# Kernel optimization log

Measured on AMD Instinct MI355X. Metric: run time of the kernel, lower is better.

The kernel has to match this reference:

```python
import jax, jax.numpy as jnp
import numpy as np

NUM_CLASSES = 128
MARGIN = 0.1
EPS = 1e-12


def setup_inputs() -> dict:
    key = jax.random.key(0)
    k1, k2, k3, k4, k5 = jax.random.split(key, 5)
    B, D = 32768, 512
    anchor = jax.random.normal(k1, (B, D), dtype=jnp.float32)
    embeddings = jax.random.normal(k2, (B, D), dtype=jnp.float32)
    # SPD inverse-covariance matrix
    A = jax.random.normal(k3, (D, D), dtype=jnp.float32) * 0.05
    cov_inv = A @ A.T + jnp.eye(D, dtype=jnp.float32)
    labels = jax.random.randint(k4, (B,), 0, NUM_CLASSES, dtype=jnp.int32)
    # negative class: deterministic stand-in for the original host-side random.choice,
    # guaranteed different from the anchor class
    offs = jax.random.randint(k5, (B,), 1, NUM_CLASSES, dtype=jnp.int32)
    neg_labels = (labels + offs) % NUM_CLASSES
    return {"anchor": anchor, "embeddings": embeddings, "cov_inv": cov_inv,
            "labels": labels, "neg_labels": neg_labels}


def _mahalanobis(diff, cov_inv):
    # diff: (B, D), cov_inv: (D, D) -> (B,)
    left = diff @ cov_inv
    d2 = jnp.sum(left * diff, axis=-1)
    return jnp.sqrt(jax.nn.relu(d2) + EPS)


def reference(anchor, embeddings, cov_inv, labels, neg_labels):
    B = embeddings.shape[0]
    # class sums / counts once via segment reduce (replaces per-sample masked means)
    sums = jax.ops.segment_sum(embeddings, labels, num_segments=NUM_CLASSES)   # (C, D)
    cnts = jax.ops.segment_sum(jnp.ones((B,), embeddings.dtype), labels,
                               num_segments=NUM_CLASSES)                        # (C,)
    # positive mean of anchor's class, excluding sample i itself
    pos_mean = (sums[labels] - embeddings) / jnp.maximum(cnts[labels] - 1.0, 1.0)[:, None]
    neg_mean = sums[neg_labels] / jnp.maximum(cnts[neg_labels], 1.0)[:, None]
    pos_d = _mahalanobis(anchor - pos_mean, cov_inv)
    neg_d = _mahalanobis(anchor - neg_mean, cov_inv)
    return jnp.mean(jax.nn.relu(pos_d - neg_d + MARGIN))
```

## Files before the change

### kernel.cpp

```cpp
#include <hip/hip_runtime.h>
#include <math.h>

#define D 512
#define C 128
#define B_TOT 32768
#define MARGIN 0.1f
#define EPS 1e-12f

typedef __attribute__((ext_vector_type(4))) short short4v;
typedef __attribute__((ext_vector_type(8))) short short8;
typedef __attribute__((ext_vector_type(16))) float f32x16;

__device__ inline unsigned short f2bf(float f) {
  union { float f; unsigned u; } v; v.f = f;
  unsigned r = v.u + 0x7fff + ((v.u >> 16) & 1);
  return (unsigned short)(r >> 16);
}
__device__ inline float bf2f(unsigned short h) {
  union { unsigned u; float f; } v; v.u = ((unsigned)h) << 16; return v.f;
}

__device__ inline void llds16(void* lds, const void* g) {
  __builtin_amdgcn_global_load_lds(
      (const __attribute__((address_space(1))) unsigned int*)g,
      (__attribute__((address_space(3))) unsigned int*)lds, 16, 0, 0);
}

__global__ __launch_bounds__(256) void prep_m(
    const float* __restrict__ M, unsigned short* __restrict__ Mh,
    float* __restrict__ Mld) {
  int p = blockIdx.x * 4 + (threadIdx.x >> 6);
  int lane = threadIdx.x & 63;
  int s = p >> 4, nt = p & 15;
  int n = nt * 32 + (lane & 31), k0 = s * 16 + (lane >> 5) * 8;
  const float4* mp4 = (const float4*)(M + (size_t)n * D + k0);
  float4 m0 = mp4[0], m1 = mp4[1];
  float mv[8] = {m0.x, m0.y, m0.z, m0.w, m1.x, m1.y, m1.z, m1.w};
  short8 hi;
#pragma unroll
  for (int j = 0; j < 8; ++j) hi[j] = (short)f2bf(mv[j]);
  *(short8*)((char*)Mh + (((size_t)p * 64 + lane) << 4)) = hi;
  if (blockIdx.x == 0) {
    for (int i = threadIdx.x; i < 512; i += 256) {
      float v = M[(size_t)i * 513];
      Mld[i] = v - bf2f(f2bf(v));
    }
  }
}

__global__ __launch_bounds__(256) void seg_part(
    const float* __restrict__ emb, const int* __restrict__ labels,
    float* __restrict__ psum, float* __restrict__ pcnt) {
  int b = blockIdx.x;
  int c = b >> 4, half = (b >> 3) & 1, slice = b & 7;
  int t = threadIdx.x, w = t >> 6, lane = t & 63;
  int col = half * 256 + w * 64 + lane;
  int r0 = slice * 4096;
  float acc = 0.f; int cnt = 0;
  int lab = labels[r0 + lane];
  for (int ch = 0; ch < 64; ++ch) {
    int nxt = (ch < 63) ? labels[r0 + (ch + 1) * 64 + lane] : 0;
    unsigned long long m = __ballot(lab == c);
    cnt += __popcll(m);
    int rb = r0 + ch * 64;
    while (m) {
      int j = __builtin_ctzll(m); m &= m - 1;
      acc += emb[(size_t)(rb + j) * D + col];
    }
    lab = nxt;
  }
  psum[(size_t)(c * 8 + slice) * D + col] = acc;
  if (half == 0 && t == 0) pcnt[c * 8 + slice] = (float)cnt;
}

__global__ __launch_bounds__(256) void seg_reduce(
    const float* __restrict__ psum, const float* __restrict__ pcnt,
    float* __restrict__ sums, float* __restrict__ cnts) {
  int c = blockIdx.x, t = threadIdx.x;
  for (int h = 0; h < 2; ++h) {
    int col = h * 256 + t;
    float s = 0.f;
#pragma unroll
    for (int sl = 0; sl < 8; ++sl) s += psum[(size_t)(c * 8 + sl) * D + col];
    sums[(size_t)c * D + col] = s;
  }
  if (t == 0) {
    float s = 0.f;
    for (int sl = 0; sl < 8; ++sl) s += pcnt[c * 8 + sl];
    cnts[c] = s;
  }
}

__global__ __launch_bounds__(256) void build_x2(
    const float* __restrict__ anchor, const float* __restrict__ emb,
    const int* __restrict__ labels, const int* __restrict__ negl,
    const float* __restrict__ sums, const float* __restrict__ cnts,
    unsigned short* __restrict__ Xfp, unsigned short* __restrict__ Xfn) {
  __shared__ float xsp[32 * 257], xsn[32 * 257];
  const int t = threadIdx.x, w = t >> 6, lane = t & 63;
  const int g = blockIdx.x;
  const int r = lane & 31, koff = (lane >> 5) * 8;

  for (int kh = 0; kh < 2; ++kh) {
    if (kh) __syncthreads();
#pragma unroll 2
    for (int it = 0; it < 8; ++it) {
      int row = it * 4 + w;
      int R = g * 32 + row;
      int lp = labels[R], ln = negl[R];
      float sp = 1.f / fmaxf(cnts[lp] - 1.f, 1.f);
      float sn = 1.f / fmaxf(cnts[ln], 1.f);
      int c0 = kh * 256 + lane * 4;
      float4 a = *(const float4*)(anchor + (size_t)R * D + c0);
      float4 e = *(const float4*)(emb + (size_t)R * D + c0);
      float4 Sp = *(const float4*)(sums + (size_t)lp * D + c0);
      float4 Sn = *(const float4*)(sums + (size_t)ln * D + c0);
      float4 xp, xn;
      xp.x = a.x - sp * (Sp.x - e.x);  xn.x = a.x - sn * Sn.x;
      xp.y = a.y - sp * (Sp.y - e.y);  xn.y = a.y - sn * Sn.y;
      xp.z = a.z - sp * (Sp.z - e.z);  xn.z = a.z - sn * Sn.z;
      xp.w = a.w - sp * (Sp.w - e.w);  xn.w = a.w - sn * Sn.w;
      *(float4*)(xsp + row * 257 + lane * 4) = xp;
      *(float4*)(xsn + row * 257 + lane * 4) = xn;
    }
    __syncthreads();
#pragma unroll
    for (int c = 0; c < 8; ++c) {
      const float* xs = (c < 4) ? xsp : xsn;
      unsigned short* Xf = (c < 4) ? Xfp : Xfn;
      int sl = w * 4 + (c & 3);
      short8 pk;
#pragma unroll
      for (int j = 0; j < 8; ++j)
        pk[j] = (short)f2bf(xs[r * 257 + sl * 16 + koff + j]);
      int s = kh * 16 + sl;
      *(short8*)((char*)Xf + ((((size_t)s * 1024 + g) * 64 + lane) << 4)) = pk;
    }
  }
}

__global__ __launch_bounds__(512, 2) void gemm_d2c(
    const unsigned short* __restrict__ Mh, const float* __restrict__ Mld,
    const unsigned short* __restrict__ Xfp, const unsigned short* __restrict__ Xfn,
    float* __restrict__ d2p) {
  __shared__ char smem[128 * 1024 + 512];
  float* MldL = (float*)(smem + 131072);
  const int t = threadIdx.x, w = t >> 6, lane = t & 63;
  const int chunk = blockIdx.x & 3, rgroup = blockIdx.x >> 2;
  const int isNeg = rgroup >> 6, rg = rgroup & 63;
  const unsigned short* Xsrc = isNeg ? Xfn : Xfp;

#pragma unroll
  for (int c = 0; c < 16; ++c) {
    int idx = w * 16 + c;
    int s = idx >> 2, ntl = idx & 3;
    llds16(smem + idx * 1024,
           (const char*)Mh + ((((size_t)(s * 16 + chunk * 4 + ntl)) * 64 + lane) << 4));
  }
  if (t < 128) MldL[t] = Mld[chunk * 128 + t];
  __syncthreads();

  const int rt0 = rg * 16 + w * 2;
  f32x16 acc[4][2];
#pragma unroll
  for (int nt = 0; nt < 4; ++nt)
#pragma unroll
    for (int rt = 0; rt < 2; ++rt)
#pragma unroll
      for (int i = 0; i < 16; ++i) acc[nt][rt][i] = 0.f;

#pragma unroll
  for (int s = 0; s < 32; ++s) {
    short8 b0 = *(const short8*)((const char*)Xsrc +
        ((((size_t)s * 1024 + rt0) * 64 + lane) << 4));
    short8 b1 = *(const short8*)((const char*)Xsrc +
        ((((size_t)s * 1024 + rt0 + 1) * 64 + lane) << 4));
    short8 a0 = *(const short8*)(smem + ((s * 4 + 0) << 10) + (lane << 4));
    short8 a1 = *(const short8*)(smem + ((s * 4 + 1) << 10) + (lane << 4));
    short8 a2 = *(const short8*)(smem + ((s * 4 + 2) << 10) + (lane << 4));
    short8 a3 = *(const short8*)(smem + ((s * 4 + 3) << 10) + (lane << 4));
    acc[0][0] = __builtin_amdgcn_mfma_f32_32x32x16_bf16(a0, b0, acc[0][0], 0, 0, 0);
    acc[0][1] = __builtin_amdgcn_mfma_f32_32x32x16_bf16(a0, b1, acc[0][1], 0, 0, 0);
    acc[1][0] = __builtin_amdgcn_mfma_f32_32x32x16_bf16(a1, b0, acc[1][0], 0, 0, 0);
    acc[1][1] = __builtin_amdgcn_mfma_f32_32x32x16_bf16(a1, b1, acc[1][1], 0, 0, 0);
    acc[2][0] = __builtin_amdgcn_mfma_f32_32x32x16_bf16(a2, b0, acc[2][0], 0, 0, 0);
    acc[2][1] = __builtin_amdgcn_mfma_f32_32x32x16_bf16(a2, b1, acc[2][1], 0, 0, 0);
    acc[3][0] = __builtin_amdgcn_mfma_f32_32x32x16_bf16(a3, b0, acc[3][0], 0, 0, 0);
    acc[3][1] = __builtin_amdgcn_mfma_f32_32x32x16_bf16(a3, b1, acc[3][1], 0, 0, 0);
  }

  const int rr = lane & 31, lh = lane >> 5;
  float d2l[2];
#pragma unroll
  for (int rt = 0; rt < 2; ++rt) {
    int rtg = rt0 + rt;
    short4v hb[4][2][2];
#pragma unroll
    for (int nt = 0; nt < 4; ++nt)
#pragma unroll
      for (int s2 = 0; s2 < 2; ++s2)
#pragma unroll
        for (int hi = 0; hi < 2; ++hi) {
          int s_h = chunk * 8 + nt * 2 + s2;
          hb[nt][s2][hi] = *(const short4v*)((const char*)Xsrc +
              ((((size_t)s_h * 1024 + rtg) * 64 + hi * 32 + rr) << 4) + lh * 8);
        }
    float d2 = 0.f;
#pragma unroll
    for (int nt = 0; nt < 4; ++nt)
#pragma unroll
      for (int i = 0; i < 16; ++i) {
        float hf = bf2f((unsigned short)hb[nt][i >> 3][(i >> 2) & 1][i & 3]);
        float mld = MldL[nt * 32 + 8 * (i >> 2) + (i & 3) + 4 * lh];
        d2 = fmaf(hf, acc[nt][rt][i] + mld * hf, d2);
      }
    d2l[rt] = d2 + __shfl_xor(d2, 32);
  }
  if (lane < 32) {
    size_t base = (size_t)chunk * 65536 + (size_t)isNeg * 32768 + rg * 512 + w * 64;
#pragma unroll
    for (int rt = 0; rt < 2; ++rt) d2p[base + rt * 32 + rr] = d2l[rt];
  }
}

__global__ __launch_bounds__(256) void loss_partial(
    const float* __restrict__ d2p, int B, float* __restrict__ partial) {
  int i = blockIdx.x * blockDim.x + threadIdx.x;
  float v = 0.f;
  if (i < B) {
    float p2 = 0.f, n2 = 0.f;
#pragma unroll
    for (int c = 0; c < 4; ++c) {
      p2 += d2p[(size_t)c * 65536 + i];
      n2 += d2p[(size_t)c * 65536 + 32768 + i];
    }
    float dp = sqrtf(fmaxf(p2, 0.f) + EPS);
    float dn = sqrtf(fmaxf(n2, 0.f) + EPS);
    v = fmaxf(dp - dn + MARGIN, 0.f);
  }
  for (int off = 32; off; off >>= 1) v += __shfl_down(v, off);
  __shared__ float ws[4];
  int w = threadIdx.x >> 6, lane = threadIdx.x & 63;
  if (lane == 0) ws[w] = v;
  __syncthreads();
  if (threadIdx.x == 0) partial[blockIdx.x] = ws[0] + ws[1] + ws[2] + ws[3];
}

__global__ __launch_bounds__(256) void loss_final(
    const float* __restrict__ partial, int n, int B, float* __restrict__ out) {
  float v = (threadIdx.x < n) ? partial[threadIdx.x] : 0.f;
  for (int off = 32; off; off >>= 1) v += __shfl_down(v, off);
  __shared__ float ws[4];
  int w = threadIdx.x >> 6, lane = threadIdx.x & 63;
  if (lane == 0) ws[w] = v;
  __syncthreads();
  if (threadIdx.x == 0) out[0] = (ws[0] + ws[1] + ws[2] + ws[3]) / (float)B;
}

extern "C" void kernel_launch(void* const* d_in, const int* in_sizes, int n_in,
                              void* d_out, int out_size, void* d_ws,
                              size_t ws_size, hipStream_t stream) {
  const float* anchor = (const float*)d_in[0];
  const float* emb = (const float*)d_in[1];
  const float* M = (const float*)d_in[2];
  const int* labels = (const int*)d_in[3];
  const int* negl = (const int*)d_in[4];

  char* ws = (char*)d_ws;
  size_t off = 0;
  auto alloc = [&](size_t bytes) {
    char* p = ws + off;
    off += (bytes + 255) & ~(size_t)255;
    return p;
  };
  unsigned short* Mh = (unsigned short*)alloc((size_t)512 * 512 * 2);
  float* Mld = (float*)alloc((size_t)512 * 4);
  float* sums = (float*)alloc((size_t)C * D * 4);
  float* cnts = (float*)alloc((size_t)C * 4);
  float* psum = (float*)alloc((size_t)C * 8 * D * 4);
  float* pcnt = (float*)alloc((size_t)C * 8 * 4);
  unsigned short* Xfp = (unsigned short*)alloc((size_t)32 * 1024 * 64 * 16);
  unsigned short* Xfn = (unsigned short*)alloc((size_t)32 * 1024 * 64 * 16);
  float* d2p = (float*)alloc((size_t)4 * 65536 * 4);
  float* lpart = (float*)alloc((size_t)(B_TOT / 256) * 4);

  prep_m<<<128, 256, 0, stream>>>(M, Mh, Mld);
  seg_part<<<2048, 256, 0, stream>>>(emb, labels, psum, pcnt);
  seg_reduce<<<128, 256, 0, stream>>>(psum, pcnt, sums, cnts);
  build_x2<<<1024, 256, 0, stream>>>(anchor, emb, labels, negl, sums, cnts, Xfp, Xfn);
  gemm_d2c<<<512, 512, 0, stream>>>(Mh, Mld, Xfp, Xfn, d2p);
  loss_partial<<<B_TOT / 256, 256, 0, stream>>>(d2p, B_TOT, lpart);
  loss_final<<<1, 256, 0, stream>>>(lpart, B_TOT / 256, B_TOT, (float*)d_out);
}
```

Measured before the change: 260.2 us.

## Stage X row tiles in LDS and stream M from global in GEMM

Reworks the d2 GEMM so each block stages a 128-row X tile (full K) in LDS, using an XOR-swizzled lane layout, and streams the matrix M from global/L2 with register double-buffering. Each block then covers the full 512 output columns instead of one of four column chunks, which removes the four-way partial d2 output and the per-chunk re-reads of X. The quadratic-form epilogue reads X from LDS and reduces across waves through shared memory. In exchange, every wave now fetches all of M from L2, and register pressure rises from the prefetch buffers.

New measurement: 254.9 us. 1.02x faster.

```diff
diff --git a/kernel.cpp b/kernel.cpp
--- a/kernel.cpp
+++ b/kernel.cpp
@@ -6,8 +6,8 @@
 #define B_TOT 32768
 #define MARGIN 0.1f
 #define EPS 1e-12f
-
-typedef __attribute__((ext_vector_type(4))) short short4v;
+#define PERM(x) ((x) ^ (((x) >> 3) & 7))
+
 typedef __attribute__((ext_vector_type(8))) short short8;
 typedef __attribute__((ext_vector_type(16))) float f32x16;
 
@@ -139,103 +139,116 @@
   }
 }
 
-__global__ __launch_bounds__(512, 2) void gemm_d2c(
+__global__ __launch_bounds__(512, 2) void gemm_d2x(
     const unsigned short* __restrict__ Mh, const float* __restrict__ Mld,
     const unsigned short* __restrict__ Xfp, const unsigned short* __restrict__ Xfn,
-    float* __restrict__ d2p) {
-  __shared__ char smem[128 * 1024 + 512];
-  float* MldL = (float*)(smem + 131072);
+    float* __restrict__ d2out) {
+  __shared__ char smem[131072];
+  __shared__ float mldl[512];
+  __shared__ float red[8][128];
   const int t = threadIdx.x, w = t >> 6, lane = t & 63;
-  const int chunk = blockIdx.x & 3, rgroup = blockIdx.x >> 2;
-  const int isNeg = rgroup >> 6, rg = rgroup & 63;
+  const int gb = blockIdx.x;
+  const int isNeg = gb >> 8, g = gb & 255;
   const unsigned short* Xsrc = isNeg ? Xfn : Xfp;
+  const int pl = PERM(lane);
 
 #pragma unroll
   for (int c = 0; c < 16; ++c) {
     int idx = w * 16 + c;
-    int s = idx >> 2, ntl = idx & 3;
+    int s = idx >> 2, rt = idx & 3;
     llds16(smem + idx * 1024,
-           (const char*)Mh + ((((size_t)(s * 16 + chunk * 4 + ntl)) * 64 + lane) << 4));
-  }
-  if (t < 128) MldL[t] = Mld[chunk * 128 + t];
+           (const char*)Xsrc + ((((size_t)s * 1024 + g * 4 + rt) * 64 + pl) << 4));
+  }
+  mldl[t] = Mld[t];
   __syncthreads();
 
-  const int rt0 = rg * 16 + w * 2;
-  f32x16 acc[4][2];
-#pragma unroll
-  for (int nt = 0; nt < 4; ++nt)
-#pragma unroll
-    for (int rt = 0; rt < 2; ++rt)
-#pragma unroll
-      for (int i = 0; i < 16; ++i) acc[nt][rt][i] = 0.f;
-
-#pragma unroll
-  for (int s = 0; s < 32; ++s) {
-    short8 b0 = *(const short8*)((const char*)Xsrc +
-        ((((size_t)s * 1024 + rt0) * 64 + lane) << 4));
-    short8 b1 = *(const short8*)((const char*)Xsrc +
-        ((((size_t)s * 1024 + rt0 + 1) * 64 + lane) << 4));
-    short8 a0 = *(const short8*)(smem + ((s * 4 + 0) << 10) + (lane << 4));
-    short8 a1 = *(const short8*)(smem + ((s * 4 + 1) << 10) + (lane << 4));
-    short8 a2 = *(const short8*)(smem + ((s * 4 + 2) << 10) + (lane << 4));
-    short8 a3 = *(const short8*)(smem + ((s * 4 + 3) << 10) + (lane << 4));
-    acc[0][0] = __builtin_amdgcn_mfma_f32_32x32x16_bf16(a0, b0, acc[0][0], 0, 0, 0);
-    acc[0][1] = __builtin_amdgcn_mfma_f32_32x32x16_bf16(a0, b1, acc[0][1], 0, 0, 0);
-    acc[1][0] = __builtin_amdgcn_mfma_f32_32x32x16_bf16(a1, b0, acc[1][0], 0, 0, 0);
-    acc[1][1] = __builtin_amdgcn_mfma_f32_32x32x16_bf16(a1, b1, acc[1][1], 0, 0, 0);
-    acc[2][0] = __builtin_amdgcn_mfma_f32_32x32x16_bf16(a2, b0, acc[2][0], 0, 0, 0);
-    acc[2][1] = __builtin_amdgcn_mfma_f32_32x32x16_bf16(a2, b1, acc[2][1], 0, 0, 0);
-    acc[3][0] = __builtin_amdgcn_mfma_f32_32x32x16_bf16(a3, b0, acc[3][0], 0, 0, 0);
-    acc[3][1] = __builtin_amdgcn_mfma_f32_32x32x16_bf16(a3, b1, acc[3][1], 0, 0, 0);
-  }
-
-  const int rr = lane & 31, lh = lane >> 5;
-  float d2l[2];
-#pragma unroll
-  for (int rt = 0; rt < 2; ++rt) {
-    int rtg = rt0 + rt;
-    short4v hb[4][2][2];
-#pragma unroll
-    for (int nt = 0; nt < 4; ++nt)
-#pragma unroll
-      for (int s2 = 0; s2 < 2; ++s2)
-#pragma unroll
-        for (int hi = 0; hi < 2; ++hi) {
-          int s_h = chunk * 8 + nt * 2 + s2;
-          hb[nt][s2][hi] = *(const short4v*)((const char*)Xsrc +
-              ((((size_t)s_h * 1024 + rtg) * 64 + hi * 32 + rr) << 4) + lh * 8);
-        }
-    float d2 = 0.f;
-#pragma unroll
-    for (int nt = 0; nt < 4; ++nt)
-#pragma unroll
-      for (int i = 0; i < 16; ++i) {
-        float hf = bf2f((unsigned short)hb[nt][i >> 3][(i >> 2) & 1][i & 3]);
-        float mld = MldL[nt * 32 + 8 * (i >> 2) + (i & 3) + 4 * lh];
-        d2 = fmaf(hf, acc[nt][rt][i] + mld * hf, d2);
+  const int lh = lane >> 5, l31 = lane & 31;
+  float d2p[4] = {0.f, 0.f, 0.f, 0.f};
+
+#pragma unroll
+  for (int ni = 0; ni < 2; ++ni) {
+    const int ntg = w * 2 + ni;
+    float mldv[16];
+#pragma unroll
+    for (int i = 0; i < 16; ++i)
+      mldv[i] = mldl[ntg * 32 + (i & 3) + 8 * (i >> 2) + 4 * lh];
+
+    f32x16 acc[4];
+#pragma unroll
+    for (int rt = 0; rt < 4; ++rt)
+#pragma unroll
+      for (int i = 0; i < 16; ++i) acc[rt][i] = 0.f;
+
+    short8 areg[4];
+#pragma unroll
+    for (int q = 0; q < 4; ++q)
+      areg[q] = *(const short8*)((const char*)Mh +
+          ((((size_t)q * 16 + ntg) * 64 + lane) << 4));
+    short8 breg[2][4];
+#pragma unroll
+    for (int rt = 0; rt < 4; ++rt)
+      breg[0][rt] = *(const short8*)(smem + (rt << 10) + (pl << 4));
+
+#pragma unroll
+    for (int s = 0; s < 32; ++s) {
+      if (s < 31) {
+#pragma unroll
+        for (int rt = 0; rt < 4; ++rt)
+          breg[(s + 1) & 1][rt] =
+              *(const short8*)(smem + (((s + 1) * 4 + rt) << 10) + (pl << 4));
       }
-    d2l[rt] = d2 + __shfl_xor(d2, 32);
-  }
+      short8 av = areg[s & 3];
+      if (s < 28)
+        areg[s & 3] = *(const short8*)((const char*)Mh +
+            ((((size_t)(s + 4) * 16 + ntg) * 64 + lane) << 4));
+#pragma unroll
+      for (int rt = 0; rt < 4; ++rt)
+        acc[rt] = __builtin_amdgcn_mfma_f32_32x32x16_bf16(av, breg[s & 1][rt],
+                                                          acc[rt], 0, 0, 0);
+    }
+
+#pragma unroll
+    for (int rt = 0; rt < 4; ++rt) {
+      float dd = 0.f;
+#pragma unroll
+      for (int i2 = 0; i2 < 8; ++i2) {
+        const int i = i2 * 2;
+        const int sh = 2 * ntg + (i >> 3);
+        const int lp = l31 + 32 * ((i >> 2) & 1);
+        const int dw = ((i & 3) >> 1) + 2 * lh;
+        unsigned u = *(const unsigned*)(smem + ((sh * 4 + rt) << 10) +
+                                        (PERM(lp) << 4) + dw * 4);
+        float hlo = bf2f((unsigned short)(u & 0xffffu));
+        float hhi = bf2f((unsigned short)(u >> 16));
+        dd = fmaf(hlo, acc[rt][i] + mldv[i] * hlo, dd);
+        dd = fmaf(hhi, acc[rt][i + 1] + mldv[i + 1] * hhi, dd);
+      }
+      d2p[rt] += dd;
+    }
+  }
+
+#pragma unroll
+  for (int rt = 0; rt < 4; ++rt) d2p[rt] += __shfl_xor(d2p[rt], 32);
   if (lane < 32) {
-    size_t base = (size_t)chunk * 65536 + (size_t)isNeg * 32768 + rg * 512 + w * 64;
-#pragma unroll
-    for (int rt = 0; rt < 2; ++rt) d2p[base + rt * 32 + rr] = d2l[rt];
+#pragma unroll
+    for (int rt = 0; rt < 4; ++rt) red[w][rt * 32 + l31] = d2p[rt];
+  }
+  __syncthreads();
+  if (t < 128) {
+    float sv = 0.f;
+#pragma unroll
+    for (int k = 0; k < 8; ++k) sv += red[k][t];
+    d2out[(size_t)isNeg * B_TOT + g * 128 + t] = sv;
   }
 }
 
 __global__ __launch_bounds__(256) void loss_partial(
-    const float* __restrict__ d2p, int B, float* __restrict__ partial) {
+    const float* __restrict__ d2, int B, float* __restrict__ partial) {
   int i = blockIdx.x * blockDim.x + threadIdx.x;
   float v = 0.f;
   if (i < B) {
-    float p2 = 0.f, n2 = 0.f;
-#pragma unroll
-    for (int c = 0; c < 4; ++c) {
-      p2 += d2p[(size_t)c * 65536 + i];
-      n2 += d2p[(size_t)c * 65536 + 32768 + i];
-    }
-    float dp = sqrtf(fmaxf(p2, 0.f) + EPS);
-    float dn = sqrtf(fmaxf(n2, 0.f) + EPS);
+    float dp = sqrtf(fmaxf(d2[i], 0.f) + EPS);
+    float dn = sqrtf(fmaxf(d2[B + i], 0.f) + EPS);
     v = fmaxf(dp - dn + MARGIN, 0.f);
   }
   for (int off = 32; off; off >>= 1) v += __shfl_down(v, off);
@@ -281,14 +294,14 @@
   float* pcnt = (float*)alloc((size_t)C * 8 * 4);
   unsigned short* Xfp = (unsigned short*)alloc((size_t)32 * 1024 * 64 * 16);
   unsigned short* Xfn = (unsigned short*)alloc((size_t)32 * 1024 * 64 * 16);
-  float* d2p = (float*)alloc((size_t)4 * 65536 * 4);
+  float* d2 = (float*)alloc((size_t)2 * B_TOT * 4);
   float* lpart = (float*)alloc((size_t)(B_TOT / 256) * 4);
 
   prep_m<<<128, 256, 0, stream>>>(M, Mh, Mld);
   seg_part<<<2048, 256, 0, stream>>>(emb, labels, psum, pcnt);
   seg_reduce<<<128, 256, 0, stream>>>(psum, pcnt, sums, cnts);
   build_x2<<<1024, 256, 0, stream>>>(anchor, emb, labels, negl, sums, cnts, Xfp, Xfn);
-  gemm_d2c<<<512, 512, 0, stream>>>(Mh, Mld, Xfp, Xfn, d2p);
-  loss_partial<<<B_TOT / 256, 256, 0, stream>>>(d2p, B_TOT, lpart);
+  gemm_d2x<<<512, 512, 0, stream>>>(Mh, Mld, Xfp, Xfn, d2);
+  loss_partial<<<B_TOT / 256, 256, 0, stream>>>(d2, B_TOT, lpart);
   loss_final<<<1, 256, 0, stream>>>(lpart, B_TOT / 256, B_TOT, (float*)d_out);
 }
```
